# Optimization experiments

Hardware: AMD Instinct MI355X
Metric: run time of the kernel (lower is better)

The kernel has to match this reference:

```python
import jax, jax.numpy as jnp
import numpy as np

N = 50000      # nodes
E = 800000     # edges (before self-loops)
F_IN = 256     # num_features
H = 8          # heads (conv1)
C = 32         # hidden_size per head (conv1)
OUT = 2        # conv2 out channels (1 head)
NEG_SLOPE = 0.2


def setup_inputs() -> dict:
    key = jax.random.key(0)
    ks = jax.random.split(key, 12)
    x = jax.random.normal(ks[0], (N, F_IN), jnp.float32)
    edge_index = jax.random.randint(ks[1], (2, E), 0, N, dtype=jnp.int64)

    def glorot(k, shape):
        fan = shape[0] if len(shape) == 2 else int(np.prod(shape))
        s = float(np.sqrt(6.0 / (fan + shape[-1])))
        return jax.random.uniform(k, shape, jnp.float32, -s, s)

    W1 = glorot(ks[2], (F_IN, H * C))
    att_src1 = glorot(ks[3], (H, C))
    att_dst1 = glorot(ks[4], (H, C))
    b1 = jnp.zeros((H * C,), jnp.float32)
    W2 = glorot(ks[5], (H * C, 1 * OUT))
    att_src2 = glorot(ks[6], (1, OUT))
    att_dst2 = glorot(ks[7], (1, OUT))
    b2 = jnp.zeros((OUT,), jnp.float32)
    return {"x": x, "edge_index": edge_index, "W1": W1, "att_src1": att_src1,
            "att_dst1": att_dst1, "b1": b1, "W2": W2, "att_src2": att_src2,
            "att_dst2": att_dst2, "b2": b2}


def gat_conv(x, src, dst, W, a_src, a_dst, b, heads, ch, n):
    # x: [n, f] -> projected [n, heads, ch]
    xp = (x @ W).reshape(n, heads, ch)
    alpha_src = jnp.einsum('nhc,hc->nh', xp, a_src)   # [n, H]
    alpha_dst = jnp.einsum('nhc,hc->nh', xp, a_dst)   # [n, H]
    e = jax.nn.leaky_relu(alpha_src[src] + alpha_dst[dst], NEG_SLOPE)  # [E', H]
    # segment softmax over edges grouped by destination node
    m = jax.ops.segment_max(e, dst, num_segments=n)                    # [n, H]
    p = jnp.exp(e - m[dst])
    denom = jax.ops.segment_sum(p, dst, num_segments=n)                # [n, H]
    alpha = p / denom[dst]                                             # [E', H]
    # weighted scatter-aggregate of source messages
    out = jax.ops.segment_sum(xp[src] * alpha[:, :, None], dst, num_segments=n)
    return out.reshape(n, heads * ch) + b


def reference(x, edge_index, W1, att_src1, att_dst1, b1, W2, att_src2, att_dst2, b2):
    n = x.shape[0]
    loops = jnp.arange(n, dtype=edge_index.dtype)  # GATConv add_self_loops=True
    src = jnp.concatenate([edge_index[0], loops])
    dst = jnp.concatenate([edge_index[1], loops])
    h = jax.nn.relu(gat_conv(x, src, dst, W1, att_src1, att_dst1, b1, H, C, n))
    # eval mode: F.dropout and attention dropout are identity
    return gat_conv(h, src, dst, W2, att_src2, att_dst2, b2, 1, OUT, n)
```

## Files before the change

### kernel.cpp

```cpp
#include <hip/hip_runtime.h>
#include <math.h>

#define N_NODES 50000
#define N_EDGES 800000
#define EP (N_EDGES + N_NODES)
#define NEG 0.2f
#define SCAN_BLOCKS 49

typedef __attribute__((ext_vector_type(8))) short bf16x8;
typedef __attribute__((ext_vector_type(4))) float f32x4;

static __device__ __forceinline__ unsigned short bf16_rn(float f) {
    union { float f; unsigned int u; } v; v.f = f;
    unsigned int u = v.u;
    unsigned int r = (u + 0x7FFFu + ((u >> 16) & 1u)) >> 16;
    return (unsigned short)r;
}
static __device__ __forceinline__ float bf16_tof(unsigned short u) {
    union { unsigned int u; float f; } v; v.u = ((unsigned int)u) << 16;
    return v.f;
}


__global__ void k_hist(const int* __restrict__ ei, int* __restrict__ counts) {
    int e = blockIdx.x * 256 + threadIdx.x;
    if (e >= EP) return;
    int d = (e < N_EDGES) ? ei[N_EDGES + e] : (e - N_EDGES);
    atomicAdd(&counts[d], 1);
}

__global__ void k_scan_block(const int* __restrict__ counts, int* __restrict__ excl,
                             int* __restrict__ bsums) {
    __shared__ int wsum[4];
    int b = blockIdx.x, t = threadIdx.x;
    int lane = t & 63, w = t >> 6;
    int i0 = b * 1024 + t * 4;
    int v0 = (i0 + 0 < N_NODES) ? counts[i0 + 0] : 0;
    int v1 = (i0 + 1 < N_NODES) ? counts[i0 + 1] : 0;
    int v2 = (i0 + 2 < N_NODES) ? counts[i0 + 2] : 0;
    int v3 = (i0 + 3 < N_NODES) ? counts[i0 + 3] : 0;
    int s = v0 + v1 + v2 + v3;
    int incl = s;
    #pragma unroll
    for (int d = 1; d < 64; d <<= 1) {
        int u = __shfl_up(incl, d);
        if (lane >= d) incl += u;
    }
    if (lane == 63) wsum[w] = incl;
    __syncthreads();
    if (t == 0) {
        int run = 0;
        #pragma unroll
        for (int i = 0; i < 4; ++i) { int x = wsum[i]; wsum[i] = run; run += x; }
        bsums[b] = run;
    }
    __syncthreads();
    int base = wsum[w] + incl - s;
    if (i0 + 0 < N_NODES) excl[i0 + 0] = base;
    if (i0 + 1 < N_NODES) excl[i0 + 1] = base + v0;
    if (i0 + 2 < N_NODES) excl[i0 + 2] = base + v0 + v1;
    if (i0 + 3 < N_NODES) excl[i0 + 3] = base + v0 + v1 + v2;
}

__global__ void k_scan_mid(int* __restrict__ bsums) {
    int t = threadIdx.x;
    int v = (t < SCAN_BLOCKS) ? bsums[t] : 0;
    int incl = v;
    #pragma unroll
    for (int d = 1; d < 64; d <<= 1) {
        int u = __shfl_up(incl, d);
        if (t >= d) incl += u;
    }
    if (t < SCAN_BLOCKS) bsums[t] = incl - v;
}

__global__ void k_scan_add(int* __restrict__ row_ptr, const int* __restrict__ bsums) {
    int b = blockIdx.x, t = threadIdx.x;
    int off = bsums[b];
    int i0 = b * 1024 + t * 4;
    #pragma unroll
    for (int j = 0; j < 4; ++j)
        if (i0 + j < N_NODES) row_ptr[i0 + j] += off;
    if (b == 0 && t == 0) row_ptr[N_NODES] = EP;
}

__global__ void k_scatter(const int* __restrict__ ei, const int* __restrict__ row_ptr,
                          int* __restrict__ fill, int* __restrict__ colb) {
    int e = blockIdx.x * 256 + threadIdx.x;
    if (e >= EP) return;
    int s, d;
    if (e < N_EDGES) { s = ei[e]; d = ei[N_EDGES + e]; }
    else             { s = e - N_EDGES; d = s; }
    int pos = row_ptr[d] + atomicAdd(&fill[d], 1);
    colb[pos] = s;
}

__global__ void k_cvtWfrag(const float* __restrict__ W1, bf16x8* __restrict__ Wfrag) {
    int ft = blockIdx.x * 256 + threadIdx.x;
    int c = ft >> 10, rem = ft & 1023;
    int nt = rem >> 6, l = rem & 63;
    int n = nt * 16 + (l & 15);
    int k0 = c * 32 + (l >> 4) * 8;
    bf16x8 f;
    #pragma unroll
    for (int j = 0; j < 8; ++j)
        f[j] = (short)bf16_rn(W1[(k0 + j) * 256 + n]);
    Wfrag[ft] = f;
}

#define GM_GRID 782
__global__ __launch_bounds__(128) void
k_gemm1m(const float* __restrict__ x, const bf16x8* __restrict__ Wfrag,
         unsigned short* __restrict__ xp1b) {
    __shared__ bf16x8 lds[1024];
    int t = threadIdx.x, l = t & 63, w = t >> 6;
    int rowbase = blockIdx.x * 64 + w * 32;
    int m = l & 15, kg = l >> 4;

    f32x4 acc0[16], acc1[16];
    #pragma unroll
    for (int nt = 0; nt < 16; ++nt) {
        acc0[nt] = (f32x4){0.f, 0.f, 0.f, 0.f};
        acc1[nt] = (f32x4){0.f, 0.f, 0.f, 0.f};
    }

    int r0 = rowbase + m;
    int r1 = rowbase + 16 + m;
    if (r0 > N_NODES - 1) r0 = N_NODES - 1;
    if (r1 > N_NODES - 1) r1 = N_NODES - 1;
    const float4* x4 = (const float4*)x;

    for (int c = 0; c < 8; ++c) {
        __syncthreads();
        const bf16x8* src = Wfrag + c * 1024;
        #pragma unroll
        for (int q = 0; q < 8; ++q)
            lds[q * 128 + t] = src[q * 128 + t];
        __syncthreads();

        int kb = (c * 32 + kg * 8) >> 2;
        float4 xa0 = x4[r0 * 64 + kb], xb0 = x4[r0 * 64 + kb + 1];
        float4 xa1 = x4[r1 * 64 + kb], xb1 = x4[r1 * 64 + kb + 1];
        bf16x8 aF0, aF1;
        aF0[0] = (short)bf16_rn(xa0.x); aF0[1] = (short)bf16_rn(xa0.y);
        aF0[2] = (short)bf16_rn(xa0.z); aF0[3] = (short)bf16_rn(xa0.w);
        aF0[4] = (short)bf16_rn(xb0.x); aF0[5] = (short)bf16_rn(xb0.y);
        aF0[6] = (short)bf16_rn(xb0.z); aF0[7] = (short)bf16_rn(xb0.w);
        aF1[0] = (short)bf16_rn(xa1.x); aF1[1] = (short)bf16_rn(xa1.y);
        aF1[2] = (short)bf16_rn(xa1.z); aF1[3] = (short)bf16_rn(xa1.w);
        aF1[4] = (short)bf16_rn(xb1.x); aF1[5] = (short)bf16_rn(xb1.y);
        aF1[6] = (short)bf16_rn(xb1.z); aF1[7] = (short)bf16_rn(xb1.w);

        #pragma unroll
        for (int nt = 0; nt < 16; ++nt) {
            bf16x8 bF = lds[nt * 64 + l];
            acc0[nt] = __builtin_amdgcn_mfma_f32_16x16x32_bf16(aF0, bF, acc0[nt], 0, 0, 0);
            acc1[nt] = __builtin_amdgcn_mfma_f32_16x16x32_bf16(aF1, bF, acc1[nt], 0, 0, 0);
        }
    }

    int cbase = l & 15, rq = l >> 4;
    #pragma unroll
    for (int reg = 0; reg < 4; ++reg) {
        int g0 = rowbase + rq * 4 + reg;
        int g1 = rowbase + 16 + rq * 4 + reg;
        if (g0 < N_NODES) {
            #pragma unroll
            for (int nt = 0; nt < 16; ++nt)
                xp1b[g0 * 256 + nt * 16 + cbase] = bf16_rn(acc0[nt][reg]);
        }
        if (g1 < N_NODES) {
            #pragma unroll
            for (int nt = 0; nt < 16; ++nt)
                xp1b[g1 * 256 + nt * 16 + cbase] = bf16_rn(acc1[nt][reg]);
        }
    }
}

__global__ void k_alphas1(const ushort4* __restrict__ xpb, const float* __restrict__ asrc,
                          const float* __restrict__ adst,
                          float* __restrict__ as1, float* __restrict__ ad1) {
    int t = threadIdx.x, l = t & 63, w = t >> 6;
    int n = blockIdx.x * 4 + w;
    ushort4 xq = xpb[n * 64 + l];
    float x0 = bf16_tof(xq.x), x1 = bf16_tof(xq.y), x2 = bf16_tof(xq.z), x3 = bf16_tof(xq.w);
    float4 a_s = ((const float4*)asrc)[l];
    float4 a_d = ((const float4*)adst)[l];
    float ds = x0 * a_s.x + x1 * a_s.y + x2 * a_s.z + x3 * a_s.w;
    float dd = x0 * a_d.x + x1 * a_d.y + x2 * a_d.z + x3 * a_d.w;
    #pragma unroll
    for (int m = 1; m < 8; m <<= 1) {
        ds += __shfl_xor(ds, m);
        dd += __shfl_xor(dd, m);
    }
    if ((l & 7) == 0) {
        int h = l >> 3;
        as1[n * 8 + h] = ds;
        ad1[n * 8 + h] = dd;
    }
}

__global__ void k_agg1(const ushort4* __restrict__ xpb, const float* __restrict__ as1,
                       const float* __restrict__ ad1, const int* __restrict__ row_ptr,
                       const int* __restrict__ colb, const float* __restrict__ b1,
                       const float* __restrict__ W2, const float* __restrict__ as2w,
                       const float* __restrict__ ad2w,
                       float* __restrict__ xp2, float* __restrict__ as2,
                       float* __restrict__ ad2) {
    int t = threadIdx.x, l = t & 63, w = t >> 6;
    int n = blockIdx.x * 4 + w;
    int hidx = l >> 3;
    float adn = ad1[n * 8 + hidx];
    int start = row_ptr[n], end = row_ptr[n + 1];
    float4 acc = {0.f, 0.f, 0.f, 0.f};
    float den = 0.f;
    int j = start;
    for (; j + 4 <= end; j += 4) {
        int s0 = colb[j], s1 = colb[j + 1], s2 = colb[j + 2], s3 = colb[j + 3];
        ushort4 x0 = xpb[s0 * 64 + l];
        ushort4 x1 = xpb[s1 * 64 + l];
        ushort4 x2 = xpb[s2 * 64 + l];
        ushort4 x3 = xpb[s3 * 64 + l];
        float e0 = as1[s0 * 8 + hidx] + adn;
        float e1 = as1[s1 * 8 + hidx] + adn;
        float e2 = as1[s2 * 8 + hidx] + adn;
        float e3 = as1[s3 * 8 + hidx] + adn;
        e0 = (e0 > 0.f) ? e0 : NEG * e0;
        e1 = (e1 > 0.f) ? e1 : NEG * e1;
        e2 = (e2 > 0.f) ? e2 : NEG * e2;
        e3 = (e3 > 0.f) ? e3 : NEG * e3;
        float p0 = __expf(e0), p1 = __expf(e1), p2 = __expf(e2), p3 = __expf(e3);
        den += (p0 + p1) + (p2 + p3);
        acc.x = fmaf(p0, bf16_tof(x0.x), acc.x);
        acc.y = fmaf(p0, bf16_tof(x0.y), acc.y);
        acc.z = fmaf(p0, bf16_tof(x0.z), acc.z);
        acc.w = fmaf(p0, bf16_tof(x0.w), acc.w);
        acc.x = fmaf(p1, bf16_tof(x1.x), acc.x);
        acc.y = fmaf(p1, bf16_tof(x1.y), acc.y);
        acc.z = fmaf(p1, bf16_tof(x1.z), acc.z);
        acc.w = fmaf(p1, bf16_tof(x1.w), acc.w);
        acc.x = fmaf(p2, bf16_tof(x2.x), acc.x);
        acc.y = fmaf(p2, bf16_tof(x2.y), acc.y);
        acc.z = fmaf(p2, bf16_tof(x2.z), acc.z);
        acc.w = fmaf(p2, bf16_tof(x2.w), acc.w);
        acc.x = fmaf(p3, bf16_tof(x3.x), acc.x);
        acc.y = fmaf(p3, bf16_tof(x3.y), acc.y);
        acc.z = fmaf(p3, bf16_tof(x3.z), acc.z);
        acc.w = fmaf(p3, bf16_tof(x3.w), acc.w);
    }
    for (; j < end; ++j) {
        int s = colb[j];
        ushort4 xv = xpb[s * 64 + l];
        float e = as1[s * 8 + hidx] + adn;
        e = (e > 0.f) ? e : NEG * e;
        float p = __expf(e);
        den += p;
        acc.x = fmaf(p, bf16_tof(xv.x), acc.x);
        acc.y = fmaf(p, bf16_tof(xv.y), acc.y);
        acc.z = fmaf(p, bf16_tof(xv.z), acc.z);
        acc.w = fmaf(p, bf16_tof(xv.w), acc.w);
    }
    float4 bv = ((const float4*)b1)[l];
    float inv = 1.f / den;
    float4 o;
    o.x = fmaxf(acc.x * inv + bv.x, 0.f);
    o.y = fmaxf(acc.y * inv + bv.y, 0.f);
    o.z = fmaxf(acc.z * inv + bv.z, 0.f);
    o.w = fmaxf(acc.w * inv + bv.w, 0.f);
    float4 wa = ((const float4*)W2)[2 * l];
    float4 wb = ((const float4*)W2)[2 * l + 1];
    float d0 = o.x * wa.x + o.y * wa.z + o.z * wb.x + o.w * wb.z;
    float d1 = o.x * wa.y + o.y * wa.w + o.z * wb.y + o.w * wb.w;
    #pragma unroll
    for (int m = 1; m < 64; m <<= 1) {
        d0 += __shfl_xor(d0, m);
        d1 += __shfl_xor(d1, m);
    }
    if (l == 0) {
        xp2[2 * n] = d0;
        xp2[2 * n + 1] = d1;
        as2[n] = d0 * as2w[0] + d1 * as2w[1];
        ad2[n] = d0 * ad2w[0] + d1 * ad2w[1];
    }
}

__global__ void k_agg2(const float* __restrict__ xp2, const float* __restrict__ as2,
                       const float* __restrict__ ad2, const int* __restrict__ row_ptr,
                       const int* __restrict__ colb, const float* __restrict__ b2,
                       float* __restrict__ out) {
    int t = threadIdx.x, l = t & 63, w = t >> 6;
    int n = blockIdx.x * 4 + w;
    int start = row_ptr[n], end = row_ptr[n + 1];
    float adn = ad2[n];
    float a0 = 0.f, a1 = 0.f, den = 0.f;
    for (int j = start + l; j < end; j += 64) {
        int s = colb[j];
        float e = as2[s] + adn;
        e = (e > 0.f) ? e : NEG * e;
        float p = __expf(e);
        den += p;
        a0 = fmaf(p, xp2[2 * s], a0);
        a1 = fmaf(p, xp2[2 * s + 1], a1);
    }
    #pragma unroll
    for (int m = 1; m < 64; m <<= 1) {
        a0 += __shfl_xor(a0, m);
        a1 += __shfl_xor(a1, m);
        den += __shfl_xor(den, m);
    }
    if (l == 0) {
        out[2 * n] = a0 / den + b2[0];
        out[2 * n + 1] = a1 / den + b2[1];
    }
}

extern "C" void kernel_launch(void* const* d_in, const int* in_sizes, int n_in,
                              void* d_out, int out_size, void* d_ws, size_t ws_size,
                              hipStream_t stream) {
    const float* x     = (const float*)d_in[0];
    const int*   ei    = (const int*)d_in[1];
    const float* W1    = (const float*)d_in[2];
    const float* asrc1 = (const float*)d_in[3];
    const float* adst1 = (const float*)d_in[4];
    const float* b1    = (const float*)d_in[5];
    const float* W2    = (const float*)d_in[6];
    const float* asrc2 = (const float*)d_in[7];
    const float* adst2 = (const float*)d_in[8];
    const float* b2    = (const float*)d_in[9];
    float* out = (float*)d_out;

    char* ws = (char*)d_ws;
    unsigned short* xp1b = (unsigned short*)(ws + 0);
    bf16x8* Wfrag  = (bf16x8*)(ws + 25600000);
    float* as1     = (float*)(ws + 102400000);
    float* ad1     = (float*)(ws + 104000000);
    float* xp2     = (float*)(ws + 105600000);
    float* as2     = (float*)(ws + 106000000);
    float* ad2     = (float*)(ws + 106200000);
    int*   counts  = (int*)  (ws + 106400000);
    int*   fill    = (int*)  (ws + 106600000);
    int*   row_ptr = (int*)  (ws + 106800000);
    int*   colb    = (int*)  (ws + 107000064);
    int*   bsums   = (int*)  (ws + 110400064);

    hipMemsetAsync(counts, 0, 400000, stream);

    int egrid = (EP + 255) / 256;
    k_hist      <<<egrid,       256, 0, stream>>>(ei, counts);
    k_scan_block<<<SCAN_BLOCKS, 256, 0, stream>>>(counts, row_ptr, bsums);
    k_scan_mid  <<<1,            64, 0, stream>>>(bsums);
    k_scan_add  <<<SCAN_BLOCKS, 256, 0, stream>>>(row_ptr, bsums);
    k_scatter   <<<egrid,       256, 0, stream>>>(ei, row_ptr, fill, colb);

    k_cvtWfrag  <<<32,     256, 0, stream>>>(W1, Wfrag);
    k_gemm1m    <<<GM_GRID, 128, 0, stream>>>(x, Wfrag, xp1b);
    k_alphas1   <<<12500,  256, 0, stream>>>((const ushort4*)xp1b, asrc1, adst1, as1, ad1);
    k_agg1      <<<12500,  256, 0, stream>>>((const ushort4*)xp1b, as1, ad1, row_ptr, colb,
                                             b1, W2, asrc2, adst2, xp2, as2, ad2);
    k_agg2      <<<12500,  256, 0, stream>>>(xp2, as2, ad2, row_ptr, colb, b2, out);
}
```

Measured before the change: 297.5 us.

## Fuse attention-logit computation into GEMM epilogue and merge scan kernels

Permutes the W1 fragment column mapping so each lane holds 16 contiguous output columns. The GEMM epilogue can then write packed 128-bit bf16 stores and compute the per-head alpha_src/alpha_dst dot products in registers, which removes the separate k_alphas1 pass that re-read xp1. The block-sum scan is folded into k_scan_add, dropping one tiny launch. The agg1 inner loop is rewritten with packed float2 bf16 unpacking to allow packed FMA, at the cost of extra epilogue register pressure in the GEMM.

```diff
diff --git a/kernel.cpp b/kernel.cpp
--- a/kernel.cpp
+++ b/kernel.cpp
@@ -9,6 +9,7 @@
 
 typedef __attribute__((ext_vector_type(8))) short bf16x8;
 typedef __attribute__((ext_vector_type(4))) float f32x4;
+typedef __attribute__((ext_vector_type(2))) float f32x2;
 
 static __device__ __forceinline__ unsigned short bf16_rn(float f) {
     union { float f; unsigned int u; } v; v.f = f;
@@ -19,6 +20,11 @@
 static __device__ __forceinline__ float bf16_tof(unsigned short u) {
     union { unsigned int u; float f; } v; v.u = ((unsigned int)u) << 16;
     return v.f;
+}
+static __device__ __forceinline__ f32x2 bf2_unpack(unsigned int u) {
+    union { unsigned int i; float f; } a, b;
+    a.i = u << 16; b.i = u & 0xFFFF0000u;
+    return (f32x2){a.f, b.f};
 }
 
 
@@ -62,21 +68,21 @@
     if (i0 + 3 < N_NODES) excl[i0 + 3] = base + v0 + v1 + v2;
 }
 
-__global__ void k_scan_mid(int* __restrict__ bsums) {
-    int t = threadIdx.x;
-    int v = (t < SCAN_BLOCKS) ? bsums[t] : 0;
-    int incl = v;
-    #pragma unroll
-    for (int d = 1; d < 64; d <<= 1) {
-        int u = __shfl_up(incl, d);
-        if (t >= d) incl += u;
-    }
-    if (t < SCAN_BLOCKS) bsums[t] = incl - v;
-}
-
 __global__ void k_scan_add(int* __restrict__ row_ptr, const int* __restrict__ bsums) {
+    __shared__ int soff;
     int b = blockIdx.x, t = threadIdx.x;
-    int off = bsums[b];
+    if (t < 64) {
+        int v = (t < SCAN_BLOCKS) ? bsums[t] : 0;
+        int incl = v;
+        #pragma unroll
+        for (int d = 1; d < 64; d <<= 1) {
+            int u = __shfl_up(incl, d);
+            if (t >= d) incl += u;
+        }
+        if (t == b) soff = incl - v;
+    }
+    __syncthreads();
+    int off = soff;
     int i0 = b * 1024 + t * 4;
     #pragma unroll
     for (int j = 0; j < 4; ++j)
@@ -99,7 +105,7 @@
     int ft = blockIdx.x * 256 + threadIdx.x;
     int c = ft >> 10, rem = ft & 1023;
     int nt = rem >> 6, l = rem & 63;
-    int n = nt * 16 + (l & 15);
+    int n = (l & 15) * 16 + nt;
     int k0 = c * 32 + (l >> 4) * 8;
     bf16x8 f;
     #pragma unroll
@@ -111,7 +117,9 @@
 #define GM_GRID 782
 __global__ __launch_bounds__(128) void
 k_gemm1m(const float* __restrict__ x, const bf16x8* __restrict__ Wfrag,
-         unsigned short* __restrict__ xp1b) {
+         unsigned short* __restrict__ xp1b,
+         const float* __restrict__ asrc, const float* __restrict__ adst,
+         float* __restrict__ as1, float* __restrict__ ad1) {
     __shared__ bf16x8 lds[1024];
     int t = threadIdx.x, l = t & 63, w = t >> 6;
     int rowbase = blockIdx.x * 64 + w * 32;
@@ -160,43 +168,41 @@
     }
 
     int cbase = l & 15, rq = l >> 4;
-    #pragma unroll
-    for (int reg = 0; reg < 4; ++reg) {
-        int g0 = rowbase + rq * 4 + reg;
-        int g1 = rowbase + 16 + rq * 4 + reg;
-        if (g0 < N_NODES) {
+    float asV[16], adV[16];
+    #pragma unroll
+    for (int q = 0; q < 4; ++q) {
+        float4 sa = ((const float4*)asrc)[cbase * 4 + q];
+        float4 da = ((const float4*)adst)[cbase * 4 + q];
+        asV[q * 4 + 0] = sa.x; asV[q * 4 + 1] = sa.y; asV[q * 4 + 2] = sa.z; asV[q * 4 + 3] = sa.w;
+        adV[q * 4 + 0] = da.x; adV[q * 4 + 1] = da.y; adV[q * 4 + 2] = da.z; adV[q * 4 + 3] = da.w;
+    }
+    #pragma unroll
+    for (int g = 0; g < 2; ++g) {
+        f32x4* A = g ? acc1 : acc0;
+        #pragma unroll
+        for (int reg = 0; reg < 4; ++reg) {
+            int gr = rowbase + g * 16 + rq * 4 + reg;
+            unsigned int ob[8];
+            float ps = 0.f, pd = 0.f;
             #pragma unroll
-            for (int nt = 0; nt < 16; ++nt)
-                xp1b[g0 * 256 + nt * 16 + cbase] = bf16_rn(acc0[nt][reg]);
+            for (int q = 0; q < 8; ++q) {
+                float v0 = A[2 * q][reg], v1 = A[2 * q + 1][reg];
+                ob[q] = (unsigned int)bf16_rn(v0) | ((unsigned int)bf16_rn(v1) << 16);
+                ps = fmaf(v0, asV[2 * q], ps);     ps = fmaf(v1, asV[2 * q + 1], ps);
+                pd = fmaf(v0, adV[2 * q], pd);     pd = fmaf(v1, adV[2 * q + 1], pd);
+            }
+            ps += __shfl_xor(ps, 1);
+            pd += __shfl_xor(pd, 1);
+            if (gr < N_NODES) {
+                uint4* dst = (uint4*)(xp1b + gr * 256 + cbase * 16);
+                dst[0] = make_uint4(ob[0], ob[1], ob[2], ob[3]);
+                dst[1] = make_uint4(ob[4], ob[5], ob[6], ob[7]);
+                if ((l & 1) == 0) {
+                    as1[gr * 8 + (cbase >> 1)] = ps;
+                    ad1[gr * 8 + (cbase >> 1)] = pd;
+                }
+            }
         }
-        if (g1 < N_NODES) {
-            #pragma unroll
-            for (int nt = 0; nt < 16; ++nt)
-                xp1b[g1 * 256 + nt * 16 + cbase] = bf16_rn(acc1[nt][reg]);
-        }
-    }
-}
-
-__global__ void k_alphas1(const ushort4* __restrict__ xpb, const float* __restrict__ asrc,
-                          const float* __restrict__ adst,
-                          float* __restrict__ as1, float* __restrict__ ad1) {
-    int t = threadIdx.x, l = t & 63, w = t >> 6;
-    int n = blockIdx.x * 4 + w;
-    ushort4 xq = xpb[n * 64 + l];
-    float x0 = bf16_tof(xq.x), x1 = bf16_tof(xq.y), x2 = bf16_tof(xq.z), x3 = bf16_tof(xq.w);
-    float4 a_s = ((const float4*)asrc)[l];
-    float4 a_d = ((const float4*)adst)[l];
-    float ds = x0 * a_s.x + x1 * a_s.y + x2 * a_s.z + x3 * a_s.w;
-    float dd = x0 * a_d.x + x1 * a_d.y + x2 * a_d.z + x3 * a_d.w;
-    #pragma unroll
-    for (int m = 1; m < 8; m <<= 1) {
-        ds += __shfl_xor(ds, m);
-        dd += __shfl_xor(dd, m);
-    }
-    if ((l & 7) == 0) {
-        int h = l >> 3;
-        as1[n * 8 + h] = ds;
-        ad1[n * 8 + h] = dd;
     }
 }
 
@@ -212,15 +218,16 @@
     int hidx = l >> 3;
     float adn = ad1[n * 8 + hidx];
     int start = row_ptr[n], end = row_ptr[n + 1];
-    float4 acc = {0.f, 0.f, 0.f, 0.f};
+    const uint2* xp2v = (const uint2*)xpb;
+    f32x2 accA = {0.f, 0.f}, accB = {0.f, 0.f};
     float den = 0.f;
     int j = start;
     for (; j + 4 <= end; j += 4) {
         int s0 = colb[j], s1 = colb[j + 1], s2 = colb[j + 2], s3 = colb[j + 3];
-        ushort4 x0 = xpb[s0 * 64 + l];
-        ushort4 x1 = xpb[s1 * 64 + l];
-        ushort4 x2 = xpb[s2 * 64 + l];
-        ushort4 x3 = xpb[s3 * 64 + l];
+        uint2 r0 = xp2v[s0 * 64 + l];
+        uint2 r1 = xp2v[s1 * 64 + l];
+        uint2 r2 = xp2v[s2 * 64 + l];
+        uint2 r3 = xp2v[s3 * 64 + l];
         float e0 = as1[s0 * 8 + hidx] + adn;
         float e1 = as1[s1 * 8 + hidx] + adn;
         float e2 = as1[s2 * 8 + hidx] + adn;
@@ -231,42 +238,30 @@
         e3 = (e3 > 0.f) ? e3 : NEG * e3;
         float p0 = __expf(e0), p1 = __expf(e1), p2 = __expf(e2), p3 = __expf(e3);
         den += (p0 + p1) + (p2 + p3);
-        acc.x = fmaf(p0, bf16_tof(x0.x), acc.x);
-        acc.y = fmaf(p0, bf16_tof(x0.y), acc.y);
-        acc.z = fmaf(p0, bf16_tof(x0.z), acc.z);
-        acc.w = fmaf(p0, bf16_tof(x0.w), acc.w);
-        acc.x = fmaf(p1, bf16_tof(x1.x), acc.x);
-        acc.y = fmaf(p1, bf16_tof(x1.y), acc.y);
-        acc.z = fmaf(p1, bf16_tof(x1.z), acc.z);
-        acc.w = fmaf(p1, bf16_tof(x1.w), acc.w);
-        acc.x = fmaf(p2, bf16_tof(x2.x), acc.x);
-        acc.y = fmaf(p2, bf16_tof(x2.y), acc.y);
-        acc.z = fmaf(p2, bf16_tof(x2.z), acc.z);
-        acc.w = fmaf(p2, bf16_tof(x2.w), acc.w);
-        acc.x = fmaf(p3, bf16_tof(x3.x), acc.x);
-        acc.y = fmaf(p3, bf16_tof(x3.y), acc.y);
-        acc.z = fmaf(p3, bf16_tof(x3.z), acc.z);
-        acc.w = fmaf(p3, bf16_tof(x3.w), acc.w);
+        f32x2 q0 = {p0, p0}, q1 = {p1, p1}, q2 = {p2, p2}, q3 = {p3, p3};
+        accA += q0 * bf2_unpack(r0.x);  accB += q0 * bf2_unpack(r0.y);
+        accA += q1 * bf2_unpack(r1.x);  accB += q1 * bf2_unpack(r1.y);
+        accA += q2 * bf2_unpack(r2.x);  accB += q2 * bf2_unpack(r2.y);
+        accA += q3 * bf2_unpack(r3.x);  accB += q3 * bf2_unpack(r3.y);
     }
     for (; j < end; ++j) {
         int s = colb[j];
-        ushort4 xv = xpb[s * 64 + l];
+        uint2 r = xp2v[s * 64 + l];
         float e = as1[s * 8 + hidx] + adn;
         e = (e > 0.f) ? e : NEG * e;
         float p = __expf(e);
         den += p;
-        acc.x = fmaf(p, bf16_tof(xv.x), acc.x);
-        acc.y = fmaf(p, bf16_tof(xv.y), acc.y);
-        acc.z = fmaf(p, bf16_tof(xv.z), acc.z);
-        acc.w = fmaf(p, bf16_tof(xv.w), acc.w);
+        f32x2 q = {p, p};
+        accA += q * bf2_unpack(r.x);
+        accB += q * bf2_unpack(r.y);
     }
     float4 bv = ((const float4*)b1)[l];
     float inv = 1.f / den;
     float4 o;
-    o.x = fmaxf(acc.x * inv + bv.x, 0.f);
-    o.y = fmaxf(acc.y * inv + bv.y, 0.f);
-    o.z = fmaxf(acc.z * inv + bv.z, 0.f);
-    o.w = fmaxf(acc.w * inv + bv.w, 0.f);
+    o.x = fmaxf(accA[0] * inv + bv.x, 0.f);
+    o.y = fmaxf(accA[1] * inv + bv.y, 0.f);
+    o.z = fmaxf(accB[0] * inv + bv.z, 0.f);
+    o.w = fmaxf(accB[1] * inv + bv.w, 0.f);
     float4 wa = ((const float4*)W2)[2 * l];
     float4 wb = ((const float4*)W2)[2 * l + 1];
     float d0 = o.x * wa.x + o.y * wa.z + o.z * wb.x + o.w * wb.z;
@@ -348,13 +343,11 @@
     int egrid = (EP + 255) / 256;
     k_hist      <<<egrid,       256, 0, stream>>>(ei, counts);
     k_scan_block<<<SCAN_BLOCKS, 256, 0, stream>>>(counts, row_ptr, bsums);
-    k_scan_mid  <<<1,            64, 0, stream>>>(bsums);
     k_scan_add  <<<SCAN_BLOCKS, 256, 0, stream>>>(row_ptr, bsums);
     k_scatter   <<<egrid,       256, 0, stream>>>(ei, row_ptr, fill, colb);
 
     k_cvtWfrag  <<<32,     256, 0, stream>>>(W1, Wfrag);
-    k_gemm1m    <<<GM_GRID, 128, 0, stream>>>(x, Wfrag, xp1b);
-    k_alphas1   <<<12500,  256, 0, stream>>>((const ushort4*)xp1b, asrc1, adst1, as1, ad1);
+    k_gemm1m    <<<GM_GRID, 128, 0, stream>>>(x, Wfrag, xp1b, asrc1, adst1, as1, ad1);
     k_agg1      <<<12500,  256, 0, stream>>>((const ushort4*)xp1b, as1, ad1, row_ptr, colb,
                                              b1, W2, asrc2, adst2, xp2, as2, ad2);
     k_agg2      <<<12500,  256, 0, stream>>>(xp2, as2, ad2, row_ptr, colb, b2, out);
```

Measured after the change: 290.6 us. -2.3%, faster.
